# Performance work log

Hardware: AMD Instinct MI355X
Metric: run time of the kernel (lower is better)

Reference implementation:

```python
import jax, jax.numpy as jnp
import numpy as np

TEMPORAL_WIDTH = 4  # hardcoded in GRUBlock


def causal_conv1d(x, w, b):
    """Depthwise causal temporal conv. x:[B,T,R], w:[4,R], b:[R].
    out[t] = sum_i w[i] * x[t - 3 + i] + b (zero left padding)."""
    T = x.shape[1]
    xp = jnp.pad(x, ((0, 0), (TEMPORAL_WIDTH - 1, 0), (0, 0)))
    y = b
    for i in range(TEMPORAL_WIDTH):  # tiny fixed loop over 4 taps
        y = y + w[i] * xp[:, i:i + T]
    return y


def linear_scan(a, b):
    """h_t = a_t * h_{t-1} + b_t with h_{-1}=0, via associative scan over time."""
    def comb(e1, e2):
        a1, b1 = e1
        a2, b2 = e2
        return a2 * a1, a2 * b1 + b2
    _, h = jax.lax.associative_scan(comb, (a, b), axis=1)
    return h


def setup_inputs() -> dict:
    key = jax.random.key(0)
    k1, k2, k3, k4 = jax.random.split(key, 4)
    B, T, H, R = 4, 8192, 1024, 1024
    x = jax.random.normal(k1, (B, T, H), dtype=jnp.float32)
    # lecun init: N(0, 1/sqrt(d_in)); torch Linear weight is [out, in]
    w_zh = jax.random.normal(k2, (2 * R, H), dtype=jnp.float32) / np.sqrt(H)
    w_out = jax.random.normal(k3, (H, R), dtype=jnp.float32) / np.sqrt(R)
    conv_w = jax.random.normal(k4, (TEMPORAL_WIDTH, R), dtype=jnp.float32) / np.sqrt(TEMPORAL_WIDTH)
    conv_b = jnp.zeros((R,), dtype=jnp.float32)
    return {"x": x, "w_zh": w_zh, "w_out": w_out, "conv_w": conv_w, "conv_b": conv_b}


def reference(x, w_zh, w_out, conv_w, conv_b):
    # residual causal conv
    x = x + causal_conv1d(x, conv_w, conv_b)
    # fused z/h projection: [B,T,H] @ [H,2R]
    zh = jnp.einsum('bth,rh->btr', x, w_zh)
    z, h = jnp.split(zh, 2, axis=-1)
    z = jax.nn.sigmoid(z)
    # GRU-style linear recurrence: h_t = (1-z_t) h_{t-1} + z_t h~_t
    h_o = linear_scan(1.0 - z, z * h)
    return jnp.einsum('btr,hr->bth', h_o, w_out)
```

## Files before the change

kernel.cpp:

```cpp
#include <hip/hip_runtime.h>

typedef __bf16 bf16x8 __attribute__((ext_vector_type(8)));
typedef __bf16 bf16x4 __attribute__((ext_vector_type(4)));
typedef float  f32x4  __attribute__((ext_vector_type(4)));
typedef float  f32x16 __attribute__((ext_vector_type(16)));

static constexpr int Bb = 4, T = 8192, H = 1024, R = 1024;
static constexpr int BT = Bb * T;
static constexpr int N1 = 2 * R;
static constexpr int CH = 64;
static constexpr int L  = T / CH;

__device__ __forceinline__ void g2lds16(const void* g, void* l) {
  __builtin_amdgcn_global_load_lds(
      (const __attribute__((address_space(1))) unsigned int*)g,
      (__attribute__((address_space(3))) unsigned int*)l, 16, 0, 0);
}

__global__ __launch_bounds__(256) void cast_f32_bf16(const float* __restrict__ in,
                                                     __bf16* __restrict__ out, int n4) {
  int i = blockIdx.x * 256 + threadIdx.x;
  if (i >= n4) return;
  const f32x4 v = *(const f32x4*)(in + (size_t)i * 4);
  bf16x4 o;
  o[0] = (__bf16)v[0]; o[1] = (__bf16)v[1]; o[2] = (__bf16)v[2]; o[3] = (__bf16)v[3];
  *(bf16x4*)(out + (size_t)i * 4) = o;
}

__global__ __launch_bounds__(256) void conv_residual_cast(const float* __restrict__ x,
                                                          const float* __restrict__ cw,
                                                          const float* __restrict__ cb,
                                                          __bf16* __restrict__ xc) {
  const size_t i4 = (size_t)blockIdx.x * 256 + threadIdx.x;
  const size_t v  = i4 * 4;
  const int    h  = (int)(v & (size_t)(H - 1));
  const size_t bt = v >> 10;
  const int    t  = (int)(bt & (size_t)(T - 1));
  f32x4 acc = *(const f32x4*)(cb + h);
  const f32x4 xv = *(const f32x4*)(x + v);
#pragma unroll
  for (int i = 0; i < 4; ++i) {
    const int tt = t - 3 + i;
    if (tt >= 0) {
      const f32x4 xi = *(const f32x4*)(x + (bt - 3 + i) * H + h);
      const f32x4 wi = *(const f32x4*)(cw + i * H + h);
      acc += wi * xi;
    }
  }
  acc += xv;
  bf16x4 o;
  o[0] = (__bf16)acc[0]; o[1] = (__bf16)acc[1]; o[2] = (__bf16)acc[2]; o[3] = (__bf16)acc[3];
  *(bf16x4*)(xc + v) = o;
}

template <typename OUT_T>
__global__ __launch_bounds__(256) void gemm_bt(const __bf16* __restrict__ A,
                                               const __bf16* __restrict__ Bm,
                                               OUT_T* __restrict__ C,
                                               int M, int N, int K) {
  __shared__ __align__(16) __bf16 sA[128 * 64];
  __shared__ __align__(16) __bf16 sB[128 * 64];
  const int tid  = threadIdx.x;
  const int wave = tid >> 6;
  const int lane = tid & 63;
  const int ln = lane & 31;
  const int kb = lane >> 5;
  const int bm0 = blockIdx.y * 128;
  const int bn0 = blockIdx.x * 128;
  const int wm = (wave >> 1) * 64;
  const int wn = (wave & 1) * 64;

  f32x16 acc[2][2] = {};

  int srow[4], sgc[4], sldsE[4];
#pragma unroll
  for (int c = 0; c < 4; ++c) {
    const int li = c * 256 + tid;
    srow[c] = li >> 3;
    sgc[c]  = (li & 7) ^ (srow[c] & 7);
    sldsE[c] = (c * 256 + (tid & ~63)) * 8;
  }

  for (int k0 = 0; k0 < K; k0 += 64) {
#pragma unroll
    for (int c = 0; c < 4; ++c) {
      g2lds16(A  + (size_t)(bm0 + srow[c]) * K + k0 + sgc[c] * 8, sA + sldsE[c]);
      g2lds16(Bm + (size_t)(bn0 + srow[c]) * K + k0 + sgc[c] * 8, sB + sldsE[c]);
    }
    __syncthreads();
#pragma unroll
    for (int ks = 0; ks < 4; ++ks) {
      bf16x8 af[2], bfr[2];
#pragma unroll
      for (int i = 0; i < 2; ++i) {
        const int ra = wm + i * 32 + ln;
        af[i]  = *(const bf16x8*)(sA + ra * 64 + (((2 * ks + kb) ^ (ra & 7)) * 8));
        const int rb = wn + i * 32 + ln;
        bfr[i] = *(const bf16x8*)(sB + rb * 64 + (((2 * ks + kb) ^ (rb & 7)) * 8));
      }
#pragma unroll
      for (int i = 0; i < 2; ++i)
#pragma unroll
        for (int j = 0; j < 2; ++j)
          acc[i][j] = __builtin_amdgcn_mfma_f32_32x32x16_bf16(af[i], bfr[j], acc[i][j], 0, 0, 0);
    }
    __syncthreads();
  }
#pragma unroll
  for (int i = 0; i < 2; ++i)
#pragma unroll
    for (int j = 0; j < 2; ++j) {
      const int col = bn0 + wn + j * 32 + ln;
#pragma unroll
      for (int rr = 0; rr < 16; ++rr) {
        const int row = bm0 + wm + i * 32 + (rr & 3) + 8 * (rr >> 2) + 4 * kb;
        C[(size_t)row * N + col] = (OUT_T)acc[i][j][rr];
      }
    }
}

__global__ __launch_bounds__(256) void scan_pass1(const __bf16* __restrict__ zh,
                                                  float* __restrict__ aggA,
                                                  float* __restrict__ aggB) {
  const int r = blockIdx.x * 256 + threadIdx.x;
  const int c = blockIdx.y;
  const int b = blockIdx.z;
  size_t base = ((size_t)b * T + (size_t)c * L) * N1 + r;
  float Aacc = 1.f, Bacc = 0.f;
#pragma unroll 4
  for (int t = 0; t < L; ++t) {
    const float s  = (float)zh[base];
    const float hh = (float)zh[base + R];
    base += N1;
    const float z = 1.f / (1.f + __expf(-s));
    const float a = 1.f - z;
    Bacc = a * Bacc + z * hh;
    Aacc *= a;
  }
  const size_t o = ((size_t)b * CH + c) * R + r;
  aggA[o] = Aacc;
  aggB[o] = Bacc;
}

__global__ __launch_bounds__(256) void scan_pass2(const float* __restrict__ aggA,
                                                  const float* __restrict__ aggB,
                                                  float* __restrict__ carry) {
  const int idx = blockIdx.x * 256 + threadIdx.x;
  const int b = idx >> 10;
  const int r = idx & (R - 1);
  float h = 0.f;
#pragma unroll 8
  for (int c = 0; c < CH; ++c) {
    const size_t o = ((size_t)b * CH + c) * R + r;
    carry[o] = h;
    h = aggA[o] * h + aggB[o];
  }
}

__global__ __launch_bounds__(256) void scan_pass3(const __bf16* __restrict__ zh,
                                                  const float* __restrict__ carry,
                                                  __bf16* __restrict__ ho) {
  const int r = blockIdx.x * 256 + threadIdx.x;
  const int c = blockIdx.y;
  const int b = blockIdx.z;
  size_t base  = ((size_t)b * T + (size_t)c * L) * N1 + r;
  size_t obase = ((size_t)b * T + (size_t)c * L) * R + r;
  float h = carry[((size_t)b * CH + c) * R + r];
#pragma unroll 4
  for (int t = 0; t < L; ++t) {
    const float s  = (float)zh[base];
    const float hh = (float)zh[base + R];
    base += N1;
    const float z = 1.f / (1.f + __expf(-s));
    h = (1.f - z) * h + z * hh;
    ho[obase] = (__bf16)h;
    obase += R;
  }
}

extern "C" void kernel_launch(void* const* d_in, const int* in_sizes, int n_in,
                              void* d_out, int out_size, void* d_ws, size_t ws_size,
                              hipStream_t stream) {
  const float* x      = (const float*)d_in[0];
  const float* w_zh   = (const float*)d_in[1];
  const float* w_out  = (const float*)d_in[2];
  const float* conv_w = (const float*)d_in[3];
  const float* conv_b = (const float*)d_in[4];
  float* out = (float*)d_out;

  char* ws = (char*)d_ws;
  size_t off = 0;
  __bf16* wzh_b  = (__bf16*)(ws + off); off += (size_t)N1 * H * 2;
  __bf16* wout_b = (__bf16*)(ws + off); off += (size_t)H * R * 2;
  __bf16* xc     = (__bf16*)(ws + off); off += (size_t)BT * H * 2;
  __bf16* zh     = (__bf16*)(ws + off); off += (size_t)BT * N1 * 2;
  float*  aggA   = (float*)(ws + off);  off += (size_t)Bb * CH * R * 4;
  float*  aggB   = (float*)(ws + off);  off += (size_t)Bb * CH * R * 4;
  float*  carry  = (float*)(ws + off);  off += (size_t)Bb * CH * R * 4;
  __bf16* ho = xc;

  cast_f32_bf16<<<(N1 * H / 4 + 255) / 256, 256, 0, stream>>>(w_zh, wzh_b, N1 * H / 4);
  cast_f32_bf16<<<(H * R / 4 + 255) / 256, 256, 0, stream>>>(w_out, wout_b, H * R / 4);
  conv_residual_cast<<<BT * H / 4 / 256, 256, 0, stream>>>(x, conv_w, conv_b, xc);
  gemm_bt<__bf16><<<dim3(N1 / 128, BT / 128), 256, 0, stream>>>(xc, wzh_b, zh, BT, N1, H);
  scan_pass1<<<dim3(R / 256, CH, Bb), 256, 0, stream>>>(zh, aggA, aggB);
  scan_pass2<<<Bb * R / 256, 256, 0, stream>>>(aggA, aggB, carry);
  scan_pass3<<<dim3(R / 256, CH, Bb), 256, 0, stream>>>(zh, carry, ho);
  gemm_bt<float><<<dim3(H / 128, BT / 128), 256, 0, stream>>>(ho, wout_b, out, BT, H, R);
}
```

Baseline: 609.3 us.

## Load GEMM B-operand directly from global, vectorize scan passes, double scan chunks

The GEMM stops staging the B (weight) tile in LDS. Each lane now reads its B fragment straight from global memory, which halves LDS use and adds a 3-blocks-per-CU occupancy hint. The scan passes now have each thread handle 4 contiguous channels with vector bf16x4 loads and stores, and the chunk count doubles to 128 to keep the grid size up. The risk is that uncached, uncoalesced global B loads inside the MFMA inner loop could stall the GEMM.

```diff
diff --git a/kernel.cpp b/kernel.cpp
--- a/kernel.cpp
+++ b/kernel.cpp
@@ -8,7 +8,7 @@
 static constexpr int Bb = 4, T = 8192, H = 1024, R = 1024;
 static constexpr int BT = Bb * T;
 static constexpr int N1 = 2 * R;
-static constexpr int CH = 64;
+static constexpr int CH = 128;
 static constexpr int L  = T / CH;
 
 __device__ __forceinline__ void g2lds16(const void* g, void* l) {
@@ -54,12 +54,11 @@
 }
 
 template <typename OUT_T>
-__global__ __launch_bounds__(256) void gemm_bt(const __bf16* __restrict__ A,
-                                               const __bf16* __restrict__ Bm,
-                                               OUT_T* __restrict__ C,
-                                               int M, int N, int K) {
+__global__ __launch_bounds__(256, 3) void gemm_bt(const __bf16* __restrict__ A,
+                                                  const __bf16* __restrict__ Bm,
+                                                  OUT_T* __restrict__ C,
+                                                  int M, int N, int K) {
   __shared__ __align__(16) __bf16 sA[128 * 64];
-  __shared__ __align__(16) __bf16 sB[128 * 64];
   const int tid  = threadIdx.x;
   const int wave = tid >> 6;
   const int lane = tid & 63;
@@ -81,22 +80,24 @@
     sldsE[c] = (c * 256 + (tid & ~63)) * 8;
   }
 
+  const __bf16* bRow0 = Bm + (size_t)(bn0 + wn + ln) * K;
+  const __bf16* bRow1 = Bm + (size_t)(bn0 + wn + 32 + ln) * K;
+
   for (int k0 = 0; k0 < K; k0 += 64) {
 #pragma unroll
-    for (int c = 0; c < 4; ++c) {
-      g2lds16(A  + (size_t)(bm0 + srow[c]) * K + k0 + sgc[c] * 8, sA + sldsE[c]);
-      g2lds16(Bm + (size_t)(bn0 + srow[c]) * K + k0 + sgc[c] * 8, sB + sldsE[c]);
-    }
+    for (int c = 0; c < 4; ++c)
+      g2lds16(A + (size_t)(bm0 + srow[c]) * K + k0 + sgc[c] * 8, sA + sldsE[c]);
     __syncthreads();
 #pragma unroll
     for (int ks = 0; ks < 4; ++ks) {
+      const int kc = (2 * ks + kb) * 8;
       bf16x8 af[2], bfr[2];
+      bfr[0] = *(const bf16x8*)(bRow0 + k0 + kc);
+      bfr[1] = *(const bf16x8*)(bRow1 + k0 + kc);
 #pragma unroll
       for (int i = 0; i < 2; ++i) {
         const int ra = wm + i * 32 + ln;
-        af[i]  = *(const bf16x8*)(sA + ra * 64 + (((2 * ks + kb) ^ (ra & 7)) * 8));
-        const int rb = wn + i * 32 + ln;
-        bfr[i] = *(const bf16x8*)(sB + rb * 64 + (((2 * ks + kb) ^ (rb & 7)) * 8));
+        af[i] = *(const bf16x8*)(sA + ra * 64 + (((2 * ks + kb) ^ (ra & 7)) * 8));
       }
 #pragma unroll
       for (int i = 0; i < 2; ++i)
@@ -122,24 +123,28 @@
 __global__ __launch_bounds__(256) void scan_pass1(const __bf16* __restrict__ zh,
                                                   float* __restrict__ aggA,
                                                   float* __restrict__ aggB) {
-  const int r = blockIdx.x * 256 + threadIdx.x;
-  const int c = blockIdx.y;
-  const int b = blockIdx.z;
-  size_t base = ((size_t)b * T + (size_t)c * L) * N1 + r;
-  float Aacc = 1.f, Bacc = 0.f;
+  const int r0 = threadIdx.x * 4;
+  const int c = blockIdx.x;
+  const int b = blockIdx.y;
+  size_t base = ((size_t)b * T + (size_t)c * L) * N1 + r0;
+  float Aacc[4] = {1.f, 1.f, 1.f, 1.f};
+  float Bacc[4] = {};
 #pragma unroll 4
   for (int t = 0; t < L; ++t) {
-    const float s  = (float)zh[base];
-    const float hh = (float)zh[base + R];
+    const bf16x4 zv = *(const bf16x4*)(zh + base);
+    const bf16x4 hv = *(const bf16x4*)(zh + base + R);
     base += N1;
-    const float z = 1.f / (1.f + __expf(-s));
-    const float a = 1.f - z;
-    Bacc = a * Bacc + z * hh;
-    Aacc *= a;
-  }
-  const size_t o = ((size_t)b * CH + c) * R + r;
-  aggA[o] = Aacc;
-  aggB[o] = Bacc;
+#pragma unroll
+    for (int e = 0; e < 4; ++e) {
+      const float z = 1.f / (1.f + __expf(-(float)zv[e]));
+      const float a = 1.f - z;
+      Bacc[e] = a * Bacc[e] + z * (float)hv[e];
+      Aacc[e] *= a;
+    }
+  }
+  const size_t o = ((size_t)b * CH + c) * R + r0;
+  *(f32x4*)(aggA + o) = *(const f32x4*)Aacc;
+  *(f32x4*)(aggB + o) = *(const f32x4*)Bacc;
 }
 
 __global__ __launch_bounds__(256) void scan_pass2(const float* __restrict__ aggA,
@@ -160,20 +165,26 @@
 __global__ __launch_bounds__(256) void scan_pass3(const __bf16* __restrict__ zh,
                                                   const float* __restrict__ carry,
                                                   __bf16* __restrict__ ho) {
-  const int r = blockIdx.x * 256 + threadIdx.x;
-  const int c = blockIdx.y;
-  const int b = blockIdx.z;
-  size_t base  = ((size_t)b * T + (size_t)c * L) * N1 + r;
-  size_t obase = ((size_t)b * T + (size_t)c * L) * R + r;
-  float h = carry[((size_t)b * CH + c) * R + r];
+  const int r0 = threadIdx.x * 4;
+  const int c = blockIdx.x;
+  const int b = blockIdx.y;
+  size_t base  = ((size_t)b * T + (size_t)c * L) * N1 + r0;
+  size_t obase = ((size_t)b * T + (size_t)c * L) * R + r0;
+  const f32x4 cv = *(const f32x4*)(carry + ((size_t)b * CH + c) * R + r0);
+  float h[4] = {cv[0], cv[1], cv[2], cv[3]};
 #pragma unroll 4
   for (int t = 0; t < L; ++t) {
-    const float s  = (float)zh[base];
-    const float hh = (float)zh[base + R];
+    const bf16x4 zv = *(const bf16x4*)(zh + base);
+    const bf16x4 hv = *(const bf16x4*)(zh + base + R);
     base += N1;
-    const float z = 1.f / (1.f + __expf(-s));
-    h = (1.f - z) * h + z * hh;
-    ho[obase] = (__bf16)h;
+    bf16x4 o;
+#pragma unroll
+    for (int e = 0; e < 4; ++e) {
+      const float z = 1.f / (1.f + __expf(-(float)zv[e]));
+      h[e] = (1.f - z) * h[e] + z * (float)hv[e];
+      o[e] = (__bf16)h[e];
+    }
+    *(bf16x4*)(ho + obase) = o;
     obase += R;
   }
 }
@@ -203,8 +214,8 @@
   cast_f32_bf16<<<(H * R / 4 + 255) / 256, 256, 0, stream>>>(w_out, wout_b, H * R / 4);
   conv_residual_cast<<<BT * H / 4 / 256, 256, 0, stream>>>(x, conv_w, conv_b, xc);
   gemm_bt<__bf16><<<dim3(N1 / 128, BT / 128), 256, 0, stream>>>(xc, wzh_b, zh, BT, N1, H);
-  scan_pass1<<<dim3(R / 256, CH, Bb), 256, 0, stream>>>(zh, aggA, aggB);
+  scan_pass1<<<dim3(CH, Bb), 256, 0, stream>>>(zh, aggA, aggB);
   scan_pass2<<<Bb * R / 256, 256, 0, stream>>>(aggA, aggB, carry);
-  scan_pass3<<<dim3(R / 256, CH, Bb), 256, 0, stream>>>(zh, carry, ho);
+  scan_pass3<<<dim3(CH, Bb), 256, 0, stream>>>(zh, carry, ho);
   gemm_bt<float><<<dim3(H / 128, BT / 128), 256, 0, stream>>>(ho, wout_b, out, BT, H, R);
 }
```

After: 779.3 us. +27.9%, slower.
